# Performance work log

Measured on AMD Instinct MI355X. Metric: run time of the kernel, lower is better.

## Reference

```python
import jax, jax.numpy as jnp
import numpy as np

WEIGHT = 1.0
BIN_SIZE = 1.0
MAX_MZ = 2000.0
NUM_BINS = int(MAX_MZ / BIN_SIZE)  # 2000
B, N = 8192, 256


def setup_inputs() -> dict:
    key = jax.random.key(0)
    k1, k2, k3, k4, k5 = jax.random.split(key, 5)
    return {
        "pred_mz": jax.random.uniform(k1, (B, N), dtype=jnp.float32),
        "pred_intensity": jax.random.uniform(k2, (B, N), dtype=jnp.float32),
        "target_mz": jax.random.uniform(k3, (B, N), dtype=jnp.float32),
        "target_intensity": jax.random.uniform(k4, (B, N), dtype=jnp.float32),
        "target_mask": jax.random.uniform(k5, (B, N), dtype=jnp.float32),
    }


def _bin_spectrum(mz, intensity):
    # mz is normalized to [0,1]; denormalize and bin. Batched scatter-add:
    # a single 2D indexed add replaces the per-sample scatter_add_ loop.
    bin_idx = jnp.clip((mz * MAX_MZ / BIN_SIZE).astype(jnp.int32), 0, NUM_BINS - 1)  # [B, N]
    bsz = mz.shape[0]
    binned = jnp.zeros((bsz, NUM_BINS), dtype=intensity.dtype)
    return binned.at[jnp.arange(bsz)[:, None], bin_idx].add(intensity)


def reference(pred_mz, pred_intensity, target_mz, target_intensity, target_mask):
    pred_binned = _bin_spectrum(pred_mz, pred_intensity)                    # [B, NUM_BINS]
    target_binned = _bin_spectrum(target_mz, target_intensity * target_mask)
    eps = 1e-8  # matches torch F.cosine_similarity default
    pn = jnp.maximum(jnp.linalg.norm(pred_binned, axis=1), eps)
    tn = jnp.maximum(jnp.linalg.norm(target_binned, axis=1), eps)
    cos = jnp.sum(pred_binned * target_binned, axis=1) / (pn * tn)
    cos = jnp.clip(cos, -1.0, 1.0)
    angle = jnp.arccos(cos)
    loss = jnp.mean(angle / jnp.pi)
    return WEIGHT * loss
```

## Files before the change

### kernel.cpp

```cpp
#include <hip/hip_runtime.h>
#include <math.h>


#define SAL_NUM_BINS 2000
#define SAL_B 8192
#define SAL_N 256

__global__ __launch_bounds__(256) void sal_row_kernel(
    const float* __restrict__ pred_mz,
    const float* __restrict__ pred_int,
    const float* __restrict__ targ_mz,
    const float* __restrict__ targ_int,
    const float* __restrict__ targ_mask,
    float* __restrict__ row_angle)
{
    __shared__ __align__(16) float hist[4][2][SAL_NUM_BINS];
    const int t = threadIdx.x;
    const int w = t >> 6;
    const int l = t & 63;
    const int row = blockIdx.x * 4 + w;
    const int base = row * SAL_N;

    const float4 pmz = ((const float4*)(pred_mz   + base))[l];
    const float4 pin = ((const float4*)(pred_int  + base))[l];
    const float4 tmz = ((const float4*)(targ_mz   + base))[l];
    const float4 ti4 = ((const float4*)(targ_int  + base))[l];
    const float4 tm4 = ((const float4*)(targ_mask + base))[l];

    {
        float4* h4 = (float4*)&hist[w][0][0];
        const float4 z = make_float4(0.f, 0.f, 0.f, 0.f);
        #pragma unroll
        for (int i = 0; i < 16; ++i) {
            int idx = l + i * 64;
            if (idx < (2 * SAL_NUM_BINS) / 4) h4[idx] = z;
        }
    }

    const float tinx = ti4.x * tm4.x, tiny_ = ti4.y * tm4.y;
    const float tinz = ti4.z * tm4.z, tinw = ti4.w * tm4.w;

    const int pb0 = min(max((int)(pmz.x * 2000.0f), 0), SAL_NUM_BINS - 1);
    const int pb1 = min(max((int)(pmz.y * 2000.0f), 0), SAL_NUM_BINS - 1);
    const int pb2 = min(max((int)(pmz.z * 2000.0f), 0), SAL_NUM_BINS - 1);
    const int pb3 = min(max((int)(pmz.w * 2000.0f), 0), SAL_NUM_BINS - 1);
    const int tb0 = min(max((int)(tmz.x * 2000.0f), 0), SAL_NUM_BINS - 1);
    const int tb1 = min(max((int)(tmz.y * 2000.0f), 0), SAL_NUM_BINS - 1);
    const int tb2 = min(max((int)(tmz.z * 2000.0f), 0), SAL_NUM_BINS - 1);
    const int tb3 = min(max((int)(tmz.w * 2000.0f), 0), SAL_NUM_BINS - 1);

    atomicAdd(&hist[w][0][pb0], pin.x);
    atomicAdd(&hist[w][0][pb1], pin.y);
    atomicAdd(&hist[w][0][pb2], pin.z);
    atomicAdd(&hist[w][0][pb3], pin.w);
    atomicAdd(&hist[w][1][tb0], tinx);
    atomicAdd(&hist[w][1][tb1], tiny_);
    atomicAdd(&hist[w][1][tb2], tinz);
    atomicAdd(&hist[w][1][tb3], tinw);

    float dot = 0.f, p2 = 0.f, t2 = 0.f;
    dot = fmaf(pin.x, hist[w][1][pb0], dot);  p2 = fmaf(pin.x, hist[w][0][pb0], p2);
    dot = fmaf(pin.y, hist[w][1][pb1], dot);  p2 = fmaf(pin.y, hist[w][0][pb1], p2);
    dot = fmaf(pin.z, hist[w][1][pb2], dot);  p2 = fmaf(pin.z, hist[w][0][pb2], p2);
    dot = fmaf(pin.w, hist[w][1][pb3], dot);  p2 = fmaf(pin.w, hist[w][0][pb3], p2);
    t2  = fmaf(tinx, hist[w][1][tb0], t2);
    t2  = fmaf(tiny_, hist[w][1][tb1], t2);
    t2  = fmaf(tinz, hist[w][1][tb2], t2);
    t2  = fmaf(tinw, hist[w][1][tb3], t2);

    #pragma unroll
    for (int off = 32; off > 0; off >>= 1) {
        dot += __shfl_down(dot, off, 64);
        p2  += __shfl_down(p2,  off, 64);
        t2  += __shfl_down(t2,  off, 64);
    }
    if (l == 0) {
        float pn = fmaxf(sqrtf(p2), 1e-8f);
        float tn = fmaxf(sqrtf(t2), 1e-8f);
        float cs = dot / (pn * tn);
        cs = fminf(fmaxf(cs, -1.0f), 1.0f);
        row_angle[row] = acosf(cs) * (float)(1.0 / M_PI);
    }
}

__global__ __launch_bounds__(256) void sal_reduce_kernel(
    const float* __restrict__ row_angle, float* __restrict__ out)
{
    const int t = threadIdx.x;
    const float4* ra4 = (const float4*)row_angle;
    float s = 0.0f;
    #pragma unroll
    for (int i = 0; i < SAL_B / 4 / 256; ++i) {
        float4 v = ra4[t + i * 256];
        s += (v.x + v.y) + (v.z + v.w);
    }
    #pragma unroll
    for (int off = 32; off > 0; off >>= 1) s += __shfl_down(s, off, 64);
    __shared__ float rbuf[4];
    if ((t & 63) == 0) rbuf[t >> 6] = s;
    __syncthreads();
    if (t == 0) out[0] = ((rbuf[0] + rbuf[1]) + (rbuf[2] + rbuf[3])) * (float)(1.0 / SAL_B);
}

extern "C" void kernel_launch(void* const* d_in, const int* in_sizes, int n_in,
                              void* d_out, int out_size, void* d_ws, size_t ws_size,
                              hipStream_t stream) {
    const float* pred_mz   = (const float*)d_in[0];
    const float* pred_int  = (const float*)d_in[1];
    const float* targ_mz   = (const float*)d_in[2];
    const float* targ_int  = (const float*)d_in[3];
    const float* targ_mask = (const float*)d_in[4];
    float* row_angle = (float*)d_ws;
    float* out = (float*)d_out;

    sal_row_kernel<<<SAL_B / 4, 256, 0, stream>>>(pred_mz, pred_int, targ_mz,
                                                  targ_int, targ_mask, row_angle);
    sal_reduce_kernel<<<1, 256, 0, stream>>>(row_angle, out);
}
```

Before: 108.4 us.

## Process two rows per wavefront, resetting only touched histogram bins between rows

Each wavefront now handles two rows instead of one and reuses its shared-memory histogram. After the first row it clears only the bins it touched, so the full 16 KB histogram is zeroed once per two rows. Per-wave partial sums of the two angles replace per-row outputs, which halves both the grid size and the work of the final reduction. In exchange, more registers are live while both rows' loads are held, and the second row's atomics are serialized behind the first row's.

```diff
diff --git a/kernel.cpp b/kernel.cpp
--- a/kernel.cpp
+++ b/kernel.cpp
@@ -6,26 +6,84 @@
 #define SAL_B 8192
 #define SAL_N 256
 
+__device__ __forceinline__ float sal_row_angle(
+    float* __restrict__ hp, float* __restrict__ hq,
+    const float4& pmz, const float4& pin,
+    const float4& tmz, const float4& tin,
+    bool undo)
+{
+    const int pb0 = min(max((int)(pmz.x * 2000.0f), 0), SAL_NUM_BINS - 1);
+    const int pb1 = min(max((int)(pmz.y * 2000.0f), 0), SAL_NUM_BINS - 1);
+    const int pb2 = min(max((int)(pmz.z * 2000.0f), 0), SAL_NUM_BINS - 1);
+    const int pb3 = min(max((int)(pmz.w * 2000.0f), 0), SAL_NUM_BINS - 1);
+    const int tb0 = min(max((int)(tmz.x * 2000.0f), 0), SAL_NUM_BINS - 1);
+    const int tb1 = min(max((int)(tmz.y * 2000.0f), 0), SAL_NUM_BINS - 1);
+    const int tb2 = min(max((int)(tmz.z * 2000.0f), 0), SAL_NUM_BINS - 1);
+    const int tb3 = min(max((int)(tmz.w * 2000.0f), 0), SAL_NUM_BINS - 1);
+
+    atomicAdd(&hp[pb0], pin.x);
+    atomicAdd(&hp[pb1], pin.y);
+    atomicAdd(&hp[pb2], pin.z);
+    atomicAdd(&hp[pb3], pin.w);
+    atomicAdd(&hq[tb0], tin.x);
+    atomicAdd(&hq[tb1], tin.y);
+    atomicAdd(&hq[tb2], tin.z);
+    atomicAdd(&hq[tb3], tin.w);
+
+    float dot = 0.f, p2 = 0.f, t2 = 0.f;
+    dot = fmaf(pin.x, hq[pb0], dot);  p2 = fmaf(pin.x, hp[pb0], p2);
+    dot = fmaf(pin.y, hq[pb1], dot);  p2 = fmaf(pin.y, hp[pb1], p2);
+    dot = fmaf(pin.z, hq[pb2], dot);  p2 = fmaf(pin.z, hp[pb2], p2);
+    dot = fmaf(pin.w, hq[pb3], dot);  p2 = fmaf(pin.w, hp[pb3], p2);
+    t2  = fmaf(tin.x, hq[tb0], t2);
+    t2  = fmaf(tin.y, hq[tb1], t2);
+    t2  = fmaf(tin.z, hq[tb2], t2);
+    t2  = fmaf(tin.w, hq[tb3], t2);
+
+    if (undo) {
+        hp[pb0] = 0.0f; hp[pb1] = 0.0f; hp[pb2] = 0.0f; hp[pb3] = 0.0f;
+        hq[tb0] = 0.0f; hq[tb1] = 0.0f; hq[tb2] = 0.0f; hq[tb3] = 0.0f;
+    }
+
+    #pragma unroll
+    for (int off = 32; off > 0; off >>= 1) {
+        dot += __shfl_down(dot, off, 64);
+        p2  += __shfl_down(p2,  off, 64);
+        t2  += __shfl_down(t2,  off, 64);
+    }
+    float pn = fmaxf(sqrtf(p2), 1e-8f);
+    float tn = fmaxf(sqrtf(t2), 1e-8f);
+    float cs = dot / (pn * tn);
+    cs = fminf(fmaxf(cs, -1.0f), 1.0f);
+    return acosf(cs) * (float)(1.0 / M_PI);
+}
+
 __global__ __launch_bounds__(256) void sal_row_kernel(
     const float* __restrict__ pred_mz,
     const float* __restrict__ pred_int,
     const float* __restrict__ targ_mz,
     const float* __restrict__ targ_int,
     const float* __restrict__ targ_mask,
-    float* __restrict__ row_angle)
+    float* __restrict__ wave_partial)
 {
     __shared__ __align__(16) float hist[4][2][SAL_NUM_BINS];
     const int t = threadIdx.x;
     const int w = t >> 6;
     const int l = t & 63;
-    const int row = blockIdx.x * 4 + w;
-    const int base = row * SAL_N;
+    const int rowA = blockIdx.x * 8 + w * 2;
+    const int baseA = rowA * SAL_N;
+    const int baseB = baseA + SAL_N;
 
-    const float4 pmz = ((const float4*)(pred_mz   + base))[l];
-    const float4 pin = ((const float4*)(pred_int  + base))[l];
-    const float4 tmz = ((const float4*)(targ_mz   + base))[l];
-    const float4 ti4 = ((const float4*)(targ_int  + base))[l];
-    const float4 tm4 = ((const float4*)(targ_mask + base))[l];
+    const float4 pmzA = ((const float4*)(pred_mz   + baseA))[l];
+    const float4 pinA = ((const float4*)(pred_int  + baseA))[l];
+    const float4 tmzA = ((const float4*)(targ_mz   + baseA))[l];
+    const float4 ti4A = ((const float4*)(targ_int  + baseA))[l];
+    const float4 tm4A = ((const float4*)(targ_mask + baseA))[l];
+    const float4 pmzB = ((const float4*)(pred_mz   + baseB))[l];
+    const float4 pinB = ((const float4*)(pred_int  + baseB))[l];
+    const float4 tmzB = ((const float4*)(targ_mz   + baseB))[l];
+    const float4 ti4B = ((const float4*)(targ_int  + baseB))[l];
+    const float4 tm4B = ((const float4*)(targ_mask + baseB))[l];
 
     {
         float4* h4 = (float4*)&hist[w][0][0];
@@ -37,61 +95,29 @@
         }
     }
 
-    const float tinx = ti4.x * tm4.x, tiny_ = ti4.y * tm4.y;
-    const float tinz = ti4.z * tm4.z, tinw = ti4.w * tm4.w;
+    float* hp = &hist[w][0][0];
+    float* hq = &hist[w][1][0];
 
-    const int pb0 = min(max((int)(pmz.x * 2000.0f), 0), SAL_NUM_BINS - 1);
-    const int pb1 = min(max((int)(pmz.y * 2000.0f), 0), SAL_NUM_BINS - 1);
-    const int pb2 = min(max((int)(pmz.z * 2000.0f), 0), SAL_NUM_BINS - 1);
-    const int pb3 = min(max((int)(pmz.w * 2000.0f), 0), SAL_NUM_BINS - 1);
-    const int tb0 = min(max((int)(tmz.x * 2000.0f), 0), SAL_NUM_BINS - 1);
-    const int tb1 = min(max((int)(tmz.y * 2000.0f), 0), SAL_NUM_BINS - 1);
-    const int tb2 = min(max((int)(tmz.z * 2000.0f), 0), SAL_NUM_BINS - 1);
-    const int tb3 = min(max((int)(tmz.w * 2000.0f), 0), SAL_NUM_BINS - 1);
+    const float4 tinA = make_float4(ti4A.x * tm4A.x, ti4A.y * tm4A.y,
+                                    ti4A.z * tm4A.z, ti4A.w * tm4A.w);
+    const float4 tinB = make_float4(ti4B.x * tm4B.x, ti4B.y * tm4B.y,
+                                    ti4B.z * tm4B.z, ti4B.w * tm4B.w);
 
-    atomicAdd(&hist[w][0][pb0], pin.x);
-    atomicAdd(&hist[w][0][pb1], pin.y);
-    atomicAdd(&hist[w][0][pb2], pin.z);
-    atomicAdd(&hist[w][0][pb3], pin.w);
-    atomicAdd(&hist[w][1][tb0], tinx);
-    atomicAdd(&hist[w][1][tb1], tiny_);
-    atomicAdd(&hist[w][1][tb2], tinz);
-    atomicAdd(&hist[w][1][tb3], tinw);
+    const float angA = sal_row_angle(hp, hq, pmzA, pinA, tmzA, tinA, true);
+    const float angB = sal_row_angle(hp, hq, pmzB, pinB, tmzB, tinB, false);
 
-    float dot = 0.f, p2 = 0.f, t2 = 0.f;
-    dot = fmaf(pin.x, hist[w][1][pb0], dot);  p2 = fmaf(pin.x, hist[w][0][pb0], p2);
-    dot = fmaf(pin.y, hist[w][1][pb1], dot);  p2 = fmaf(pin.y, hist[w][0][pb1], p2);
-    dot = fmaf(pin.z, hist[w][1][pb2], dot);  p2 = fmaf(pin.z, hist[w][0][pb2], p2);
-    dot = fmaf(pin.w, hist[w][1][pb3], dot);  p2 = fmaf(pin.w, hist[w][0][pb3], p2);
-    t2  = fmaf(tinx, hist[w][1][tb0], t2);
-    t2  = fmaf(tiny_, hist[w][1][tb1], t2);
-    t2  = fmaf(tinz, hist[w][1][tb2], t2);
-    t2  = fmaf(tinw, hist[w][1][tb3], t2);
-
-    #pragma unroll
-    for (int off = 32; off > 0; off >>= 1) {
-        dot += __shfl_down(dot, off, 64);
-        p2  += __shfl_down(p2,  off, 64);
-        t2  += __shfl_down(t2,  off, 64);
-    }
-    if (l == 0) {
-        float pn = fmaxf(sqrtf(p2), 1e-8f);
-        float tn = fmaxf(sqrtf(t2), 1e-8f);
-        float cs = dot / (pn * tn);
-        cs = fminf(fmaxf(cs, -1.0f), 1.0f);
-        row_angle[row] = acosf(cs) * (float)(1.0 / M_PI);
-    }
+    if (l == 0) wave_partial[blockIdx.x * 4 + w] = angA + angB;
 }
 
 __global__ __launch_bounds__(256) void sal_reduce_kernel(
-    const float* __restrict__ row_angle, float* __restrict__ out)
+    const float* __restrict__ wave_partial, float* __restrict__ out)
 {
     const int t = threadIdx.x;
-    const float4* ra4 = (const float4*)row_angle;
+    const float4* wp4 = (const float4*)wave_partial;
     float s = 0.0f;
     #pragma unroll
-    for (int i = 0; i < SAL_B / 4 / 256; ++i) {
-        float4 v = ra4[t + i * 256];
+    for (int i = 0; i < 4096 / 4 / 256; ++i) {
+        float4 v = wp4[t + i * 256];
         s += (v.x + v.y) + (v.z + v.w);
     }
     #pragma unroll
@@ -110,10 +136,10 @@
     const float* targ_mz   = (const float*)d_in[2];
     const float* targ_int  = (const float*)d_in[3];
     const float* targ_mask = (const float*)d_in[4];
-    float* row_angle = (float*)d_ws;
+    float* wave_partial = (float*)d_ws;
     float* out = (float*)d_out;
 
-    sal_row_kernel<<<SAL_B / 4, 256, 0, stream>>>(pred_mz, pred_int, targ_mz,
-                                                  targ_int, targ_mask, row_angle);
-    sal_reduce_kernel<<<1, 256, 0, stream>>>(row_angle, out);
+    sal_row_kernel<<<SAL_B / 8, 256, 0, stream>>>(pred_mz, pred_int, targ_mz,
+                                                  targ_int, targ_mask, wave_partial);
+    sal_reduce_kernel<<<1, 256, 0, stream>>>(wave_partial, out);
 }
```

Result: faster. 105.3 us (-2.9%).
